# Kernel optimization log

Measured on AMD Instinct MI355X. Metric: run time of the kernel, lower is better.

## Reference

```python
import jax, jax.numpy as jnp
import numpy as np

N_HEADS = 16
N_KV_HEADS = 4
HEAD_DIM = 128


def _rope(x, cos, sin):
    # x: [b, s, h, d]; cos/sin: [s, d//2]; interleaved pair rotation
    b, s, h, d = x.shape
    xp = x.reshape(b, s, h, d // 2, 2)
    x_r, x_i = xp[..., 0], xp[..., 1]
    c = cos[None, :, None, :]
    sn = sin[None, :, None, :]
    o_r = x_r * c - x_i * sn
    o_i = x_r * sn + x_i * c
    return jnp.stack([o_r, o_i], axis=-1).reshape(b, s, h, d)


def setup_inputs() -> dict:
    key = jax.random.key(0)
    ks = jax.random.split(key, 7)
    B, S, D = 2, 2048, 2048
    KV = N_KV_HEADS * HEAD_DIM
    x = jax.random.normal(ks[0], (B, S, D), dtype=jnp.float32)
    freqs_cos = jax.random.uniform(ks[1], (S, HEAD_DIM // 2), dtype=jnp.float32)
    freqs_sin = jax.random.uniform(ks[2], (S, HEAD_DIM // 2), dtype=jnp.float32)
    scale = 0.02
    wq = jax.random.normal(ks[3], (D, D), dtype=jnp.float32) * scale
    wk = jax.random.normal(ks[4], (KV, D), dtype=jnp.float32) * scale
    wv = jax.random.normal(ks[5], (KV, D), dtype=jnp.float32) * scale
    wo = jax.random.normal(ks[6], (D, D), dtype=jnp.float32) * scale
    return {"x": x, "freqs_cos": freqs_cos, "freqs_sin": freqs_sin,
            "wq": wq, "wk": wk, "wv": wv, "wo": wo}


def reference(x, freqs_cos, freqs_sin, wq, wk, wv, wo):
    B, S, D = x.shape
    n_rep = N_HEADS // N_KV_HEADS
    q = (x @ wq.T).reshape(B, S, N_HEADS, HEAD_DIM)
    k = (x @ wk.T).reshape(B, S, N_KV_HEADS, HEAD_DIM)
    v = (x @ wv.T).reshape(B, S, N_KV_HEADS, HEAD_DIM)
    q = _rope(q, freqs_cos, freqs_sin)
    k = _rope(k, freqs_cos, freqs_sin)
    # repeat_kv == torch.repeat_interleave along head dim
    k = jnp.repeat(k, n_rep, axis=2)
    v = jnp.repeat(v, n_rep, axis=2)
    q = q.transpose(0, 2, 1, 3)  # [B, H, S, d]
    k = k.transpose(0, 2, 1, 3)
    v = v.transpose(0, 2, 1, 3)
    scale = 1.0 / np.sqrt(HEAD_DIM).astype(np.float32)
    scores = jnp.einsum('bhqd,bhkd->bhqk', q, k) * scale
    causal = jnp.tril(jnp.ones((S, S), dtype=bool))
    scores = jnp.where(causal[None, None], scores, jnp.finfo(jnp.float32).min)
    probs = jax.nn.softmax(scores.astype(jnp.float32), axis=-1).astype(q.dtype)
    out = jnp.einsum('bhqk,bhkd->bhqd', probs, v)
    out = out.transpose(0, 2, 1, 3).reshape(B, S, N_HEADS * HEAD_DIM)
    return out @ wo.T
```

## Files before the change

### kernel.cpp

```cpp
#include <hip/hip_runtime.h>
#include <hip/hip_bf16.h>
#include <type_traits>

using bf16x8 = __attribute__((ext_vector_type(8))) short;
using f32x4  = __attribute__((ext_vector_type(4))) float;
using u16x8  = __attribute__((ext_vector_type(8))) unsigned short;
using u16x4  = __attribute__((ext_vector_type(4))) unsigned short;
using u32x4  = __attribute__((ext_vector_type(4))) unsigned int;

__device__ __forceinline__ float b2f(unsigned short u) {
    unsigned int x = ((unsigned int)u) << 16;
    return __builtin_bit_cast(float, x);
}
__device__ __forceinline__ unsigned short f2b(float f) {
    __hip_bfloat16 h = __float2bfloat16(f);
    return __builtin_bit_cast(unsigned short, h);
}

#if defined(__has_builtin)
#if __has_builtin(__builtin_amdgcn_exp2f)
#define EXP2F(x) __builtin_amdgcn_exp2f(x)
#else
#define EXP2F(x) exp2f(x)
#endif
#else
#define EXP2F(x) exp2f(x)
#endif

__device__ __forceinline__ void async_copy16(const void* g, void* l) {
    __builtin_amdgcn_global_load_lds(
        (const __attribute__((address_space(1))) unsigned int*)g,
        (__attribute__((address_space(3))) unsigned int*)l, 16, 0, 0);
}

#define MFMA16(a, b, c) __builtin_amdgcn_mfma_f32_16x16x32_bf16(a, b, c, 0, 0, 0)

#define BARRIER() do { asm volatile("" ::: "memory"); \
    __builtin_amdgcn_s_barrier(); asm volatile("" ::: "memory"); } while (0)
#define VMCNT6() asm volatile("s_waitcnt vmcnt(6)" ::: "memory")
#define VMCNT0() asm volatile("s_waitcnt vmcnt(0)" ::: "memory")

__global__ __launch_bounds__(256) void cvt_f32_to_bf16(
    const float* __restrict__ s, unsigned short* __restrict__ d, int n4)
{
    int i = blockIdx.x * blockDim.x + threadIdx.x;
    if (i >= n4) return;
    float4 v = ((const float4*)s)[i];
    ushort4 o;
    o.x = f2b(v.x); o.y = f2b(v.y); o.z = f2b(v.z); o.w = f2b(v.w);
    ((ushort4*)d)[i] = o;
}

__global__ __launch_bounds__(512, 2) void qkv_gemm(
    const unsigned short* __restrict__ A,
    const unsigned short* __restrict__ Wq,
    const unsigned short* __restrict__ Wk,
    const unsigned short* __restrict__ Wv,
    unsigned short* __restrict__ Q,
    unsigned short* __restrict__ Kk,
    unsigned short* __restrict__ V)
{
    const int K = 2048;
    __shared__ unsigned short ldsA[2][256 * 64];
    __shared__ unsigned short ldsB[2][256 * 64];

    int tid  = threadIdx.x;
    int w    = tid >> 6;
    int lane = tid & 63;
    int idx  = lane & 15;
    int quad = lane >> 4;
    int srow   = lane >> 3;
    int schunk = (lane & 7) ^ srow;

    int wfm = (w >> 2) * 64;
    int wfn = (w & 3) * 64;

    int bid = (blockIdx.x & 7) * 24 + (blockIdx.x >> 3);
    int bm = bid / 12;
    int bn = bid - bm * 12;
    int m0 = bm * 256;

    const unsigned short* Bt;
    unsigned short* C;
    int Nc, n0;
    if (bn < 8)       { Bt = Wq + (size_t)bn * 256 * K;        C = Q;  Nc = 2048; n0 = bn * 256; }
    else if (bn < 10) { Bt = Wk + (size_t)(bn - 8) * 256 * K;  C = Kk; Nc = 512;  n0 = (bn - 8) * 256; }
    else              { Bt = Wv + (size_t)(bn - 10) * 256 * K; C = V;  Nc = 512;  n0 = (bn - 10) * 256; }

    const unsigned short* Ab = A + (size_t)m0 * K;

    f32x4 acc[8][4];
    #pragma unroll
    for (int mf = 0; mf < 8; ++mf)
        #pragma unroll
        for (int nf = 0; nf < 4; ++nf) acc[mf][nf] = (f32x4){0.f, 0.f, 0.f, 0.f};

    bf16x8 a[4][2], b0[2][2], b1[2][2];

    auto STAGE = [&](const unsigned short* __restrict__ G, int rb, int kc,
                     unsigned short* dst) {
        #pragma unroll
        for (int i = 0; i < 2; ++i) {
            int R = (w * 2 + i) * 8;
            async_copy16(G + (size_t)(rb + R + srow) * K + kc + schunk * 8,
                         dst + (size_t)R * 64);
        }
    };
    auto LDA = [&](int d, int mh) {
        #pragma unroll
        for (int mi = 0; mi < 4; ++mi) {
            int r = mh * 128 + wfm + mi * 16 + idx;
            #pragma unroll
            for (int ks = 0; ks < 2; ++ks)
                a[mi][ks] = *(const bf16x8*)&ldsA[d][r * 64 + (((ks * 4 + quad) ^ (r & 7)) << 3)];
        }
    };
    auto LDB0 = [&](int d, int nh) {
        #pragma unroll
        for (int nj = 0; nj < 2; ++nj) {
            int r = wfn + nh * 32 + nj * 16 + idx;
            #pragma unroll
            for (int ks = 0; ks < 2; ++ks)
                b0[nj][ks] = *(const bf16x8*)&ldsB[d][r * 64 + (((ks * 4 + quad) ^ (r & 7)) << 3)];
        }
    };
    auto LDB1 = [&](int d, int nh) {
        #pragma unroll
        for (int nj = 0; nj < 2; ++nj) {
            int r = wfn + nh * 32 + nj * 16 + idx;
            #pragma unroll
            for (int ks = 0; ks < 2; ++ks)
                b1[nj][ks] = *(const bf16x8*)&ldsB[d][r * 64 + (((ks * 4 + quad) ^ (r & 7)) << 3)];
        }
    };
    auto MM0 = [&](int mh, int nh) {
        __builtin_amdgcn_s_setprio(1);
        #pragma unroll
        for (int mi = 0; mi < 4; ++mi)
            #pragma unroll
            for (int nj = 0; nj < 2; ++nj)
                #pragma unroll
                for (int ks = 0; ks < 2; ++ks)
                    acc[mh * 4 + mi][nh * 2 + nj] =
                        MFMA16(a[mi][ks], b0[nj][ks], acc[mh * 4 + mi][nh * 2 + nj]);
        __builtin_amdgcn_s_setprio(0);
    };
    auto MM1 = [&](int mh, int nh) {
        __builtin_amdgcn_s_setprio(1);
        #pragma unroll
        for (int mi = 0; mi < 4; ++mi)
            #pragma unroll
            for (int nj = 0; nj < 2; ++nj)
                #pragma unroll
                for (int ks = 0; ks < 2; ++ks)
                    acc[mh * 4 + mi][nh * 2 + nj] =
                        MFMA16(a[mi][ks], b1[nj][ks], acc[mh * 4 + mi][nh * 2 + nj]);
        __builtin_amdgcn_s_setprio(0);
    };

    STAGE(Ab, 0,   0,  &ldsA[0][0]);
    STAGE(Ab, 128, 0,  &ldsA[0][128 * 64]);
    STAGE(Bt, 0,   0,  &ldsB[0][0]);
    STAGE(Bt, 128, 0,  &ldsB[0][128 * 64]);
    STAGE(Ab, 0,   64, &ldsA[1][0]);
    STAGE(Bt, 0,   64, &ldsB[1][0]);
    STAGE(Bt, 128, 64, &ldsB[1][128 * 64]);
    VMCNT6();
    BARRIER();

    for (int it = 0; it < 15; ++it) {
        int u = 2 * it;
        LDA(0, 0); LDB0(0, 0);
        STAGE(Ab, 128, (u + 1) * 64, &ldsA[1][128 * 64]);
        BARRIER(); MM0(0, 0); BARRIER();
        LDB1(0, 1);
        STAGE(Ab, 0, (u + 2) * 64, &ldsA[0][0]);
        BARRIER(); MM1(0, 1); BARRIER();
        LDA(0, 1);
        STAGE(Bt, 0, (u + 2) * 64, &ldsB[0][0]);
        BARRIER(); MM1(1, 1); BARRIER();
        STAGE(Bt, 128, (u + 2) * 64, &ldsB[0][128 * 64]);
        VMCNT6();
        BARRIER(); MM0(1, 0); BARRIER();
        LDA(1, 0); LDB0(1, 0);
        STAGE(Ab, 128, (u + 2) * 64, &ldsA[0][128 * 64]);
        BARRIER(); MM0(0, 0); BARRIER();
        LDB1(1, 1);
        STAGE(Ab, 0, (u + 3) * 64, &ldsA[1][0]);
        BARRIER(); MM1(0, 1); BARRIER();
        LDA(1, 1);
        STAGE(Bt, 0, (u + 3) * 64, &ldsB[1][0]);
        BARRIER(); MM1(1, 1); BARRIER();
        STAGE(Bt, 128, (u + 3) * 64, &ldsB[1][128 * 64]);
        VMCNT6();
        BARRIER(); MM0(1, 0); BARRIER();
    }

    LDA(0, 0); LDB0(0, 0);
    STAGE(Ab, 128, 31 * 64, &ldsA[1][128 * 64]);
    BARRIER(); MM0(0, 0); BARRIER();
    LDB1(0, 1);
    BARRIER(); MM1(0, 1); BARRIER();
    LDA(0, 1);
    BARRIER(); MM1(1, 1); BARRIER();
    VMCNT0();
    BARRIER(); MM0(1, 0); BARRIER();
    LDA(1, 0); LDB0(1, 0);
    BARRIER(); MM0(0, 0); BARRIER();
    LDB1(1, 1);
    BARRIER(); MM1(0, 1); BARRIER();
    LDA(1, 1);
    BARRIER(); MM1(1, 1); BARRIER();
    MM0(1, 0);

    #pragma unroll
    for (int mf = 0; mf < 8; ++mf) {
        #pragma unroll
        for (int r = 0; r < 4; ++r) {
            size_t row = (size_t)(m0 + (mf >> 2) * 128 + wfm + (mf & 3) * 16 + quad * 4 + r);
            #pragma unroll
            for (int nf = 0; nf < 4; ++nf) {
                int col = n0 + wfn + nf * 16 + idx;
                C[row * Nc + col] = f2b(acc[mf][nf][r]);
            }
        }
    }
}

__device__ __forceinline__ void g_stage(
    const unsigned short* __restrict__ A, const unsigned short* __restrict__ Bt,
    unsigned short* As, unsigned short* Bs,
    int k0, int K, int w, int srow, int schunk)
{
    #pragma unroll
    for (int i = 0; i < 4; ++i) {
        int cb = w * 4 + i;
        size_t goff = (size_t)(cb * 8 + srow) * K + k0 + schunk * 8;
        async_copy16(A  + goff, &As[cb * 512]);
        async_copy16(Bt + goff, &Bs[cb * 512]);
    }
}
__device__ __forceinline__ void g_compute(
    const unsigned short* As, const unsigned short* Bs,
    f32x4 (&acc)[4][4], int wm, int wn, int idx, int quad)
{
    #pragma unroll
    for (int ks = 0; ks < 2; ++ks) {
        bf16x8 af[4], bfr[4];
        #pragma unroll
        for (int mi = 0; mi < 4; ++mi) {
            int row = wm + mi * 16 + idx;
            af[mi] = *(const bf16x8*)&As[row * 64 + (((ks * 4 + quad) ^ (row & 7)) * 8)];
        }
        #pragma unroll
        for (int ni = 0; ni < 4; ++ni) {
            int row = wn + ni * 16 + idx;
            bfr[ni] = *(const bf16x8*)&Bs[row * 64 + (((ks * 4 + quad) ^ (row & 7)) * 8)];
        }
        #pragma unroll
        for (int mi = 0; mi < 4; ++mi)
            #pragma unroll
            for (int ni = 0; ni < 4; ++ni)
                acc[mi][ni] = MFMA16(af[mi], bfr[ni], acc[mi][ni]);
    }
}

template <typename OutT>
__global__ __launch_bounds__(256) void gemm_tile(
    const unsigned short* __restrict__ A,
    const unsigned short* __restrict__ Bt,
    OutT* __restrict__ C,
    int M, int N, int K)
{
    constexpr int BK = 64;
    __shared__ unsigned short As0[128 * BK];
    __shared__ unsigned short Bs0[128 * BK];
    __shared__ unsigned short As1[128 * BK];
    __shared__ unsigned short Bs1[128 * BK];

    int tid  = threadIdx.x;
    int w    = tid >> 6;
    int lane = tid & 63;
    int idx  = lane & 15;
    int quad = lane >> 4;
    int wm   = (w >> 1) * 64;
    int wn   = (w & 1) * 64;

    int tilesN = N / 128;
    int bm = blockIdx.x / tilesN;
    int bn = blockIdx.x - bm * tilesN;
    int m0 = bm * 128, n0 = bn * 128;

    const unsigned short* Ab = A  + (size_t)m0 * K;
    const unsigned short* Bb = Bt + (size_t)n0 * K;

    int srow   = lane >> 3;
    int schunk = (lane & 7) ^ srow;

    f32x4 acc[4][4];
    #pragma unroll
    for (int mi = 0; mi < 4; ++mi)
        #pragma unroll
        for (int ni = 0; ni < 4; ++ni) acc[mi][ni] = (f32x4){0.f, 0.f, 0.f, 0.f};

    g_stage(Ab, Bb, As0, Bs0, 0, K, w, srow, schunk);
    __syncthreads();

    for (int k0 = 0; k0 < K; k0 += 2 * BK) {
        if (k0 + BK < K)
            g_stage(Ab, Bb, As1, Bs1, k0 + BK, K, w, srow, schunk);
        g_compute(As0, Bs0, acc, wm, wn, idx, quad);
        __syncthreads();
        if (k0 + 2 * BK < K)
            g_stage(Ab, Bb, As0, Bs0, k0 + 2 * BK, K, w, srow, schunk);
        g_compute(As1, Bs1, acc, wm, wn, idx, quad);
        __syncthreads();
    }

    #pragma unroll
    for (int mi = 0; mi < 4; ++mi) {
        #pragma unroll
        for (int r = 0; r < 4; ++r) {
            size_t row = (size_t)(m0 + wm + mi * 16 + quad * 4 + r);
            #pragma unroll
            for (int ni = 0; ni < 4; ++ni) {
                int col = n0 + wn + ni * 16 + idx;
                if constexpr (std::is_same_v<OutT, float>) {
                    C[row * N + col] = acc[mi][ni][r];
                } else {
                    C[row * N + col] = f2b(acc[mi][ni][r]);
                }
            }
        }
    }
}

__global__ __launch_bounds__(256) void rope_kernel(
    unsigned short* __restrict__ x,
    const float* __restrict__ cs,
    const float* __restrict__ sn,
    int H, int total, float oscale)
{
    int e = blockIdx.x * blockDim.x + threadIdx.x;
    if (e >= total) return;
    int i = e & 63;
    int s = (e / (64 * H)) & 2047;
    float xr = b2f(x[2 * e]);
    float xi = b2f(x[2 * e + 1]);
    float c  = cs[s * 64 + i];
    float sv = sn[s * 64 + i];
    x[2 * e]     = f2b((xr * c - xi * sv) * oscale);
    x[2 * e + 1] = f2b((xr * sv + xi * c) * oscale);
}

__global__ __launch_bounds__(512, 4) void flash_attn(
    const unsigned short* __restrict__ qg,
    const unsigned short* __restrict__ kk,
    const unsigned short* __restrict__ vv,
    unsigned short* __restrict__ out)
{
    const int S = 2048;
    int bid = blockIdx.x;
    int qp  = bid & 15;
    int bh  = bid >> 4;
    int h   = bh & 15;
    int b   = bh >> 4;
    int kvh = h >> 2;

    int p   = b ? (15 - qp) : qp;

    int tid  = threadIdx.x;
    int w    = tid >> 6;
    int lane = tid & 63;
    int idx  = lane & 15;
    int quad = lane >> 4;

    int qt  = 2 * p + (w >> 2);
    int q0  = qt * 64;
    int wq0 = q0 + (w & 3) * 16;
    int qr  = wq0 + idx;

    __shared__ unsigned short Ks[2][32 * 128];
    __shared__ unsigned short Vt[2][128 * 40];

    const unsigned short* kbase = kk + ((size_t)b * S * 4 + kvh) * 128;
    const unsigned short* vbase = vv + ((size_t)b * S * 4 + kvh) * 128;

    bf16x8 qf[4];
    {
        const unsigned short* qpp =
            qg + ((size_t)((b * S + wq0 + idx) * 16 + h)) * 128 + quad * 8;
        #pragma unroll
        for (int ko = 0; ko < 4; ++ko)
            qf[ko] = *(const bf16x8*)(qpp + ko * 32);
    }

    f32x4 acc[8];
    #pragma unroll
    for (int n = 0; n < 8; ++n) acc[n] = (f32x4){0.f, 0.f, 0.f, 0.f};
    float lsum = 0.f;

    int s_   = w & 3;
    int vr   = (w >> 2) * 64 + lane;
    int vodd = lane & 1;
    int cpb  = vr & ~1;
    int vwoff = vr * 40 + ((s_ ^ ((vr >> 3) & 3)) << 3);

    int key = w * 4 + (lane >> 4);
    int ksc = (lane & 15) ^ (key & 7);

    int nt = 4 * p + 4;

    unsigned int vld[4];

    auto STAGE_ISSUE = [&](int t, int d) {
        async_copy16(kbase + ((size_t)(t * 32 + key)) * 512 + ksc * 8,
                     &Ks[d][w * 512]);
        const unsigned short* vc = vbase + ((size_t)t * 32) * 512 + cpb;
        #pragma unroll
        for (int i = 0; i < 4; ++i) {
            int ii = vodd * 4 + i;
            int gk = s_ * 4 + (ii >> 1) + 16 * (ii & 1);
            vld[i] = *(const unsigned int*)(vc + (size_t)gk * 512);
        }
    };
    auto STAGE_WRITE = [&](int d) {
        unsigned int L01 = (vld[0] & 0xffffu) | (vld[1] << 16);
        unsigned int L23 = (vld[2] & 0xffffu) | (vld[3] << 16);
        unsigned int H01 = (vld[0] >> 16) | (vld[1] & 0xffff0000u);
        unsigned int H23 = (vld[2] >> 16) | (vld[3] & 0xffff0000u);
        unsigned int x0 = vodd ? L01 : H01;
        unsigned int x1 = vodd ? L23 : H23;
        unsigned int y0 = __shfl_xor(x0, 1);
        unsigned int y1 = __shfl_xor(x1, 1);
        u32x4 row;
        if (vodd) row = (u32x4){y0, y1, H01, H23};
        else      row = (u32x4){L01, L23, y0, y1};
        *(u32x4*)&Vt[d][vwoff] = row;
    };

    STAGE_ISSUE(0, 0);
    VMCNT0();
    STAGE_WRITE(0);
    __syncthreads();

    for (int t = 0; t < nt; ++t) {
        int bc = t & 1;
        if (t + 1 < nt) STAGE_ISSUE(t + 1, bc ^ 1);

        if (t * 32 <= wq0 + 15) {
            f32x4 s0 = {0.f,0.f,0.f,0.f}, s1 = {0.f,0.f,0.f,0.f};
            #pragma unroll
            for (int ko = 0; ko < 4; ++ko) {
                int kc = ko * 4 + quad;
                bf16x8 kf0 = *(const bf16x8*)&Ks[bc][idx * 128 + ((kc ^ (idx & 7)) * 8)];
                bf16x8 kf1 = *(const bf16x8*)&Ks[bc][(16 + idx) * 128 + ((kc ^ (idx & 7)) * 8)];
                s0 = MFMA16(kf0, qf[ko], s0);
                s1 = MFMA16(kf1, qf[ko], s1);
            }
            unsigned int pk[4];
            if (t * 32 + 31 <= wq0) {
                #pragma unroll
                for (int r = 0; r < 4; ++r) {
                    float p0 = EXP2F(s0[r]);
                    float p1 = EXP2F(s1[r]);
                    lsum += p0 + p1;
                    pk[r] = (unsigned int)f2b(p0) | ((unsigned int)f2b(p1) << 16);
                }
            } else {
                int L = qr - t * 32;
                #pragma unroll
                for (int r = 0; r < 4; ++r) {
                    int kl = quad * 4 + r;
                    float p0 = (kl      <= L) ? EXP2F(s0[r]) : 0.f;
                    float p1 = (kl + 16 <= L) ? EXP2F(s1[r]) : 0.f;
                    lsum += p0 + p1;
                    pk[r] = (unsigned int)f2b(p0) | ((unsigned int)f2b(p1) << 16);
                }
            }
            u32x4 pku = {pk[0], pk[1], pk[2], pk[3]};
            bf16x8 pf = __builtin_bit_cast(bf16x8, pku);
            #pragma unroll
            for (int n = 0; n < 8; ++n) {
                int rr = n * 16 + idx;
                bf16x8 vf = *(const bf16x8*)&Vt[bc][rr * 40 + ((quad ^ ((rr >> 3) & 3)) << 3)];
                acc[n] = MFMA16(vf, pf, acc[n]);
            }
        }

        if (t + 1 < nt) {
            VMCNT0();
            STAGE_WRITE(bc ^ 1);
        }
        __syncthreads();
    }

    lsum += __shfl_xor(lsum, 16);
    lsum += __shfl_xor(lsum, 32);
    float inv = 1.f / lsum;
    size_t rowb = (size_t)(b * S + wq0 + idx) * 2048 + h * 128;
    #pragma unroll
    for (int n = 0; n < 8; ++n) {
        ushort4 o;
        o.x = f2b(acc[n][0] * inv);
        o.y = f2b(acc[n][1] * inv);
        o.z = f2b(acc[n][2] * inv);
        o.w = f2b(acc[n][3] * inv);
        *(ushort4*)&out[rowb + n * 16 + quad * 4] = o;
    }
}

extern "C" void kernel_launch(void* const* d_in, const int* in_sizes, int n_in,
                              void* d_out, int out_size, void* d_ws, size_t ws_size,
                              hipStream_t stream)
{
    const float* x  = (const float*)d_in[0];
    const float* fc = (const float*)d_in[1];
    const float* fs = (const float*)d_in[2];
    const float* wq = (const float*)d_in[3];
    const float* wk = (const float*)d_in[4];
    const float* wv = (const float*)d_in[5];
    const float* wo = (const float*)d_in[6];
    float* out = (float*)d_out;

    const int B = 2, S = 2048, D = 2048, KV = 512;
    const int M = B * S;

    unsigned short* ws  = (unsigned short*)d_ws;
    unsigned short* xb  = ws;
    unsigned short* wqb = xb  + (size_t)M * D;
    unsigned short* wkb = wqb + (size_t)D * D;
    unsigned short* wvb = wkb + (size_t)KV * D;
    unsigned short* wob = wvb + (size_t)KV * D;
    unsigned short* qb  = wob + (size_t)D * D;
    unsigned short* kb  = qb  + (size_t)M * D;
    unsigned short* vb  = kb  + (size_t)M * KV;
    unsigned short* ao  = vb  + (size_t)M * KV;

    cvt_f32_to_bf16<<<dim3((M * D / 4) / 256), dim3(256), 0, stream>>>(x,  xb,  M * D / 4);
    cvt_f32_to_bf16<<<dim3((D * D / 4) / 256), dim3(256), 0, stream>>>(wq, wqb, D * D / 4);
    cvt_f32_to_bf16<<<dim3((KV * D / 4) / 256), dim3(256), 0, stream>>>(wk, wkb, KV * D / 4);
    cvt_f32_to_bf16<<<dim3((KV * D / 4) / 256), dim3(256), 0, stream>>>(wv, wvb, KV * D / 4);
    cvt_f32_to_bf16<<<dim3((D * D / 4) / 256), dim3(256), 0, stream>>>(wo, wob, D * D / 4);

    qkv_gemm<<<dim3(192), dim3(512), 0, stream>>>(xb, wqb, wkb, wvb, qb, kb, vb);

    int qpairs = B * S * 16 * 64;
    int kpairs = B * S * 4 * 64;
    const float c2 = 0.12752584f;
    rope_kernel<<<dim3(qpairs / 256), dim3(256), 0, stream>>>(qb, fc, fs, 16, qpairs, c2);
    rope_kernel<<<dim3(kpairs / 256), dim3(256), 0, stream>>>(kb, fc, fs, 4, kpairs, 1.0f);

    flash_attn<<<dim3(512), dim3(512), 0, stream>>>(qb, kb, vb, ao);

    gemm_tile<float><<<dim3((M / 128) * (D / 128)), dim3(256), 0, stream>>>(ao, wob, out, M, D, D);
}
```

Before: 317.6 us.

## Have each flash-attention wave process 32 query rows, halving block size

The flash attention block shrinks from 8 waves to 4. Each wave now handles two 16-row query sub-tiles that share every K and V fragment read from LDS, which halves LDS traffic per unit of MFMA work. The K/V staging loop is rewritten so that 4 waves load the same 32-key tile, each thread issuing more loads, and the V transpose no longer needs lane shuffles. The cost is higher register use per wave for the doubled accumulators and fewer waves available to hide latency.

```diff
diff --git a/kernel.cpp b/kernel.cpp
--- a/kernel.cpp
+++ b/kernel.cpp
@@ -353,7 +353,7 @@
     x[2 * e + 1] = f2b((xr * sv + xi * c) * oscale);
 }
 
-__global__ __launch_bounds__(512, 4) void flash_attn(
+__global__ __launch_bounds__(256, 2) void flash_attn(
     const unsigned short* __restrict__ qg,
     const unsigned short* __restrict__ kk,
     const unsigned short* __restrict__ vv,
@@ -375,10 +375,9 @@
     int idx  = lane & 15;
     int quad = lane >> 4;
 
-    int qt  = 2 * p + (w >> 2);
-    int q0  = qt * 64;
-    int wq0 = q0 + (w & 3) * 16;
-    int qr  = wq0 + idx;
+    int qt  = 2 * p + (w >> 1);
+    int wq0 = qt * 64 + (w & 1) * 32;
+    int qrA = wq0 + idx;
 
     __shared__ unsigned short Ks[2][32 * 128];
     __shared__ unsigned short Vt[2][128 * 40];
@@ -386,57 +385,59 @@
     const unsigned short* kbase = kk + ((size_t)b * S * 4 + kvh) * 128;
     const unsigned short* vbase = vv + ((size_t)b * S * 4 + kvh) * 128;
 
-    bf16x8 qf[4];
+    bf16x8 qfA[4], qfB[4];
     {
-        const unsigned short* qpp =
+        const unsigned short* qa =
             qg + ((size_t)((b * S + wq0 + idx) * 16 + h)) * 128 + quad * 8;
-        #pragma unroll
-        for (int ko = 0; ko < 4; ++ko)
-            qf[ko] = *(const bf16x8*)(qpp + ko * 32);
-    }
-
-    f32x4 acc[8];
-    #pragma unroll
-    for (int n = 0; n < 8; ++n) acc[n] = (f32x4){0.f, 0.f, 0.f, 0.f};
-    float lsum = 0.f;
-
-    int s_   = w & 3;
-    int vr   = (w >> 2) * 64 + lane;
-    int vodd = lane & 1;
-    int cpb  = vr & ~1;
-    int vwoff = vr * 40 + ((s_ ^ ((vr >> 3) & 3)) << 3);
-
-    int key = w * 4 + (lane >> 4);
-    int ksc = (lane & 15) ^ (key & 7);
+        const unsigned short* qb2 =
+            qg + ((size_t)((b * S + wq0 + 16 + idx) * 16 + h)) * 128 + quad * 8;
+        #pragma unroll
+        for (int ko = 0; ko < 4; ++ko) {
+            qfA[ko] = *(const bf16x8*)(qa  + ko * 32);
+            qfB[ko] = *(const bf16x8*)(qb2 + ko * 32);
+        }
+    }
+
+    f32x4 accA[8], accB[8];
+    #pragma unroll
+    for (int n = 0; n < 8; ++n) {
+        accA[n] = (f32x4){0.f, 0.f, 0.f, 0.f};
+        accB[n] = (f32x4){0.f, 0.f, 0.f, 0.f};
+    }
+    float lsumA = 0.f, lsumB = 0.f;
+
+    int key0 = w * 8 + (lane >> 4);
+    int ksc0 = (lane & 15) ^ (key0 & 7);
+    int ksc1 = (lane & 15) ^ ((key0 + 4) & 7);
+
+    int dp = lane * 2;
+    int swzslot = ((w ^ ((dp >> 3) & 3)) << 3);
 
     int nt = 4 * p + 4;
 
-    unsigned int vld[4];
+    unsigned int vld[8];
 
     auto STAGE_ISSUE = [&](int t, int d) {
-        async_copy16(kbase + ((size_t)(t * 32 + key)) * 512 + ksc * 8,
-                     &Ks[d][w * 512]);
-        const unsigned short* vc = vbase + ((size_t)t * 32) * 512 + cpb;
-        #pragma unroll
-        for (int i = 0; i < 4; ++i) {
-            int ii = vodd * 4 + i;
-            int gk = s_ * 4 + (ii >> 1) + 16 * (ii & 1);
-            vld[i] = *(const unsigned int*)(vc + (size_t)gk * 512);
+        async_copy16(kbase + ((size_t)(t * 32 + key0)) * 512 + ksc0 * 8,
+                     &Ks[d][(w * 8) * 128]);
+        async_copy16(kbase + ((size_t)(t * 32 + key0 + 4)) * 512 + ksc1 * 8,
+                     &Ks[d][(w * 8 + 4) * 128]);
+        const unsigned short* vc = vbase + ((size_t)(t * 32 + w * 4)) * 512 + dp;
+        #pragma unroll
+        for (int ii = 0; ii < 8; ++ii) {
+            int gk = (ii >> 1) + 16 * (ii & 1);
+            vld[ii] = *(const unsigned int*)(vc + (size_t)gk * 512);
         }
     };
     auto STAGE_WRITE = [&](int d) {
-        unsigned int L01 = (vld[0] & 0xffffu) | (vld[1] << 16);
-        unsigned int L23 = (vld[2] & 0xffffu) | (vld[3] << 16);
-        unsigned int H01 = (vld[0] >> 16) | (vld[1] & 0xffff0000u);
-        unsigned int H23 = (vld[2] >> 16) | (vld[3] & 0xffff0000u);
-        unsigned int x0 = vodd ? L01 : H01;
-        unsigned int x1 = vodd ? L23 : H23;
-        unsigned int y0 = __shfl_xor(x0, 1);
-        unsigned int y1 = __shfl_xor(x1, 1);
-        u32x4 row;
-        if (vodd) row = (u32x4){y0, y1, H01, H23};
-        else      row = (u32x4){L01, L23, y0, y1};
-        *(u32x4*)&Vt[d][vwoff] = row;
+        u16x8 lo, hi;
+        #pragma unroll
+        for (int ii = 0; ii < 8; ++ii) {
+            lo[ii] = (unsigned short)vld[ii];
+            hi[ii] = (unsigned short)(vld[ii] >> 16);
+        }
+        *(u16x8*)&Vt[d][dp * 40 + swzslot]       = lo;
+        *(u16x8*)&Vt[d][(dp + 1) * 40 + swzslot] = hi;
     };
 
     STAGE_ISSUE(0, 0);
@@ -448,43 +449,56 @@
         int bc = t & 1;
         if (t + 1 < nt) STAGE_ISSUE(t + 1, bc ^ 1);
 
-        if (t * 32 <= wq0 + 15) {
-            f32x4 s0 = {0.f,0.f,0.f,0.f}, s1 = {0.f,0.f,0.f,0.f};
+        if (t * 32 <= wq0 + 31) {
+            f32x4 s0A = {0.f,0.f,0.f,0.f}, s1A = {0.f,0.f,0.f,0.f};
+            f32x4 s0B = {0.f,0.f,0.f,0.f}, s1B = {0.f,0.f,0.f,0.f};
             #pragma unroll
             for (int ko = 0; ko < 4; ++ko) {
                 int kc = ko * 4 + quad;
                 bf16x8 kf0 = *(const bf16x8*)&Ks[bc][idx * 128 + ((kc ^ (idx & 7)) * 8)];
                 bf16x8 kf1 = *(const bf16x8*)&Ks[bc][(16 + idx) * 128 + ((kc ^ (idx & 7)) * 8)];
-                s0 = MFMA16(kf0, qf[ko], s0);
-                s1 = MFMA16(kf1, qf[ko], s1);
+                s0A = MFMA16(kf0, qfA[ko], s0A);
+                s1A = MFMA16(kf1, qfA[ko], s1A);
+                s0B = MFMA16(kf0, qfB[ko], s0B);
+                s1B = MFMA16(kf1, qfB[ko], s1B);
             }
-            unsigned int pk[4];
+            unsigned int pkA[4], pkB[4];
             if (t * 32 + 31 <= wq0) {
                 #pragma unroll
                 for (int r = 0; r < 4; ++r) {
-                    float p0 = EXP2F(s0[r]);
-                    float p1 = EXP2F(s1[r]);
-                    lsum += p0 + p1;
-                    pk[r] = (unsigned int)f2b(p0) | ((unsigned int)f2b(p1) << 16);
+                    float a0 = EXP2F(s0A[r]), a1 = EXP2F(s1A[r]);
+                    float b0_ = EXP2F(s0B[r]), b1_ = EXP2F(s1B[r]);
+                    lsumA += a0 + a1;
+                    lsumB += b0_ + b1_;
+                    pkA[r] = (unsigned int)f2b(a0) | ((unsigned int)f2b(a1) << 16);
+                    pkB[r] = (unsigned int)f2b(b0_) | ((unsigned int)f2b(b1_) << 16);
                 }
             } else {
-                int L = qr - t * 32;
+                int LA = qrA - t * 32;
+                int LB = LA + 16;
                 #pragma unroll
                 for (int r = 0; r < 4; ++r) {
                     int kl = quad * 4 + r;
-                    float p0 = (kl      <= L) ? EXP2F(s0[r]) : 0.f;
-                    float p1 = (kl + 16 <= L) ? EXP2F(s1[r]) : 0.f;
-                    lsum += p0 + p1;
-                    pk[r] = (unsigned int)f2b(p0) | ((unsigned int)f2b(p1) << 16);
+                    float a0 = (kl      <= LA) ? EXP2F(s0A[r]) : 0.f;
+                    float a1 = (kl + 16 <= LA) ? EXP2F(s1A[r]) : 0.f;
+                    float b0_ = (kl      <= LB) ? EXP2F(s0B[r]) : 0.f;
+                    float b1_ = (kl + 16 <= LB) ? EXP2F(s1B[r]) : 0.f;
+                    lsumA += a0 + a1;
+                    lsumB += b0_ + b1_;
+                    pkA[r] = (unsigned int)f2b(a0) | ((unsigned int)f2b(a1) << 16);
+                    pkB[r] = (unsigned int)f2b(b0_) | ((unsigned int)f2b(b1_) << 16);
                 }
             }
-            u32x4 pku = {pk[0], pk[1], pk[2], pk[3]};
-            bf16x8 pf = __builtin_bit_cast(bf16x8, pku);
+            u32x4 pkuA = {pkA[0], pkA[1], pkA[2], pkA[3]};
+            u32x4 pkuB = {pkB[0], pkB[1], pkB[2], pkB[3]};
+            bf16x8 pfA = __builtin_bit_cast(bf16x8, pkuA);
+            bf16x8 pfB = __builtin_bit_cast(bf16x8, pkuB);
             #pragma unroll
             for (int n = 0; n < 8; ++n) {
                 int rr = n * 16 + idx;
                 bf16x8 vf = *(const bf16x8*)&Vt[bc][rr * 40 + ((quad ^ ((rr >> 3) & 3)) << 3)];
-                acc[n] = MFMA16(vf, pf, acc[n]);
+                accA[n] = MFMA16(vf, pfA, accA[n]);
+                accB[n] = MFMA16(vf, pfB, accB[n]);
             }
         }
 
@@ -495,18 +509,27 @@
         __syncthreads();
     }
 
-    lsum += __shfl_xor(lsum, 16);
-    lsum += __shfl_xor(lsum, 32);
-    float inv = 1.f / lsum;
-    size_t rowb = (size_t)(b * S + wq0 + idx) * 2048 + h * 128;
+    lsumA += __shfl_xor(lsumA, 16);
+    lsumA += __shfl_xor(lsumA, 32);
+    lsumB += __shfl_xor(lsumB, 16);
+    lsumB += __shfl_xor(lsumB, 32);
+    float invA = 1.f / lsumA;
+    float invB = 1.f / lsumB;
+    size_t rowA = (size_t)(b * S + wq0 + idx) * 2048 + h * 128;
+    size_t rowB = rowA + (size_t)16 * 2048;
     #pragma unroll
     for (int n = 0; n < 8; ++n) {
-        ushort4 o;
-        o.x = f2b(acc[n][0] * inv);
-        o.y = f2b(acc[n][1] * inv);
-        o.z = f2b(acc[n][2] * inv);
-        o.w = f2b(acc[n][3] * inv);
-        *(ushort4*)&out[rowb + n * 16 + quad * 4] = o;
+        ushort4 oA, oB;
+        oA.x = f2b(accA[n][0] * invA);
+        oA.y = f2b(accA[n][1] * invA);
+        oA.z = f2b(accA[n][2] * invA);
+        oA.w = f2b(accA[n][3] * invA);
+        oB.x = f2b(accB[n][0] * invB);
+        oB.y = f2b(accB[n][1] * invB);
+        oB.z = f2b(accB[n][2] * invB);
+        oB.w = f2b(accB[n][3] * invB);
+        *(ushort4*)&out[rowA + n * 16 + quad * 4] = oA;
+        *(ushort4*)&out[rowB + n * 16 + quad * 4] = oB;
     }
 }
 
@@ -551,7 +574,7 @@
     rope_kernel<<<dim3(qpairs / 256), dim3(256), 0, stream>>>(qb, fc, fs, 16, qpairs, c2);
     rope_kernel<<<dim3(kpairs / 256), dim3(256), 0, stream>>>(kb, fc, fs, 4, kpairs, 1.0f);
 
-    flash_attn<<<dim3(512), dim3(512), 0, stream>>>(qb, kb, vb, ao);
+    flash_attn<<<dim3(512), dim3(256), 0, stream>>>(qb, kb, vb, ao);
 
     gemm_tile<float><<<dim3((M / 128) * (D / 128)), dim3(256), 0, stream>>>(ao, wob, out, M, D, D);
 }
```

Measured after the change: 315.9 us. Within noise of the previous version (-0.5%).
